# Kernel optimization log

Measured on AMD Instinct MI355X. Metric: run time of the kernel, lower is better.

## Reference

```python
import jax, jax.numpy as jnp
import numpy as np

V = 50000
E = 500000
D = 128


def setup_inputs() -> dict:
    key = jax.random.key(0)
    k1, k2, k3, k4, k5, k6 = jax.random.split(key, 6)
    edge_feats = jax.random.normal(k1, (E, D), dtype=jnp.float32)
    node_feats = jax.random.normal(k2, (V, 1), dtype=jnp.float32)
    edge_index = jax.random.randint(k3, (2, E), 0, V, dtype=jnp.int64)
    rev_index = jax.random.randint(k4, (E,), 0, E, dtype=jnp.int64)
    # Linear(hidden_dim, hidden_dim, bias=True) params, Kaiming-uniform-ish init
    lim = 1.0 / np.sqrt(D)
    W = jax.random.uniform(k5, (D, D), dtype=jnp.float32, minval=-lim, maxval=lim)
    b = jax.random.uniform(k6, (D,), dtype=jnp.float32, minval=-lim, maxval=lim)
    return {"edge_feats": edge_feats, "node_feats": node_feats, "W": W, "b": b,
            "edge_index": edge_index, "rev_index": rev_index}


def reference(edge_feats, node_feats, W, b, edge_index, rev_index):
    src, dest = edge_index[0], edge_index[1]
    messages = jax.nn.relu(edge_feats)                      # [E, d]
    # scatter-sum messages onto destination nodes
    node_messages = jax.ops.segment_sum(messages, dest, num_segments=node_feats.shape[0])  # [V, d]
    # gather back to edges, subtract reverse-edge message (D-MPNN)
    edge_messages = node_messages[src] - messages[rev_index]  # [E, d]
    # update: Linear (dropout p=0.0 is identity)
    return edge_messages @ W.T + b
```

## Files before the change

kernel.cpp:

```cpp
#include <hip/hip_runtime.h>

#define DD 128
#define TILE_E 64

typedef __attribute__((ext_vector_type(8))) short short8;
typedef __attribute__((ext_vector_type(4))) float f32x4;

__device__ __forceinline__ unsigned short f2bf(float f) {
  unsigned int u = __float_as_uint(f);
  u += 0x7FFF + ((u >> 16) & 1);
  return (unsigned short)(u >> 16);
}


__global__ __launch_bounds__(256) void hist_kernel(
    const int* __restrict__ eidx, int* __restrict__ cnt, int E) {
  int e = blockIdx.x * 256 + threadIdx.x;
  if (e < E) atomicAdd(&cnt[eidx[E + e]], 1);
}

__global__ __launch_bounds__(1024) void scan_kernel(
    const int* __restrict__ cnt, int* __restrict__ off, int* __restrict__ cur, int V) {
  __shared__ int s[1024];
  const int t = threadIdx.x;
  const int chunk = (V + 1023) / 1024;
  const int lo = t * chunk, hi = min(lo + chunk, V);
  int tot = 0;
  for (int v = lo; v < hi; ++v) tot += cnt[v];
  s[t] = tot;
  __syncthreads();
  for (int d = 1; d < 1024; d <<= 1) {
    int x = (t >= d) ? s[t - d] : 0;
    __syncthreads();
    s[t] += x;
    __syncthreads();
  }
  int run = (t > 0) ? s[t - 1] : 0;
  for (int v = lo; v < hi; ++v) {
    off[v] = run; cur[v] = run;
    run += cnt[v];
  }
}

__global__ __launch_bounds__(256) void fill_kernel(
    const int* __restrict__ eidx, int* __restrict__ cur,
    int* __restrict__ elist, int E) {
  int e = blockIdx.x * 256 + threadIdx.x;
  if (e < E) {
    int p = atomicAdd(&cur[eidx[E + e]], 1);
    elist[p] = e;
  }
}

__global__ __launch_bounds__(256) void gather_sum_kernel(
    const float* __restrict__ ef, const int* __restrict__ off,
    const int* __restrict__ cnt, const int* __restrict__ elist,
    float* __restrict__ nm, int V) {
  const int lane = threadIdx.x & 63;
  const int half = lane >> 5;
  const int l32  = lane & 31;
  const int v = blockIdx.x * 4 + (threadIdx.x >> 6);
  if (v >= V) return;
  const int base = off[v];
  const int deg  = cnt[v];
  f32x4 acc = (f32x4){0.f, 0.f, 0.f, 0.f};
  if (deg > 0) {
    const int esafe = elist[base];
    for (int j = 0; j < deg; j += 16) {
      int idx[8];
      #pragma unroll
      for (int i = 0; i < 8; ++i) {
        int sl = j + 2 * i + half;
        idx[i] = (sl < deg) ? elist[base + sl] : esafe;
      }
      const float* p0 = ef + (size_t)idx[0] * DD + l32 * 4;
      const float* p1 = ef + (size_t)idx[1] * DD + l32 * 4;
      const float* p2 = ef + (size_t)idx[2] * DD + l32 * 4;
      const float* p3 = ef + (size_t)idx[3] * DD + l32 * 4;
      const float* p4 = ef + (size_t)idx[4] * DD + l32 * 4;
      const float* p5 = ef + (size_t)idx[5] * DD + l32 * 4;
      const float* p6 = ef + (size_t)idx[6] * DD + l32 * 4;
      const float* p7 = ef + (size_t)idx[7] * DD + l32 * 4;
      float4 m0, m1, m2, m3, m4, m5, m6, m7;
      asm volatile(
          "global_load_dwordx4 %0, %8, off\n\t"
          "global_load_dwordx4 %1, %9, off\n\t"
          "global_load_dwordx4 %2, %10, off\n\t"
          "global_load_dwordx4 %3, %11, off\n\t"
          "global_load_dwordx4 %4, %12, off\n\t"
          "global_load_dwordx4 %5, %13, off\n\t"
          "global_load_dwordx4 %6, %14, off\n\t"
          "global_load_dwordx4 %7, %15, off"
          : "=&v"(m0), "=&v"(m1), "=&v"(m2), "=&v"(m3),
            "=&v"(m4), "=&v"(m5), "=&v"(m6), "=&v"(m7)
          : "v"(p0), "v"(p1), "v"(p2), "v"(p3),
            "v"(p4), "v"(p5), "v"(p6), "v"(p7)
          : "memory");
      asm volatile("s_waitcnt vmcnt(0)" ::: "memory");
      __builtin_amdgcn_sched_barrier(0);
      #pragma unroll
      for (int i = 0; i < 8; ++i) {
        float4 m;
        switch (i) {
          case 0: m = m0; break; case 1: m = m1; break;
          case 2: m = m2; break; case 3: m = m3; break;
          case 4: m = m4; break; case 5: m = m5; break;
          case 6: m = m6; break; default: m = m7; break;
        }
        int sl = j + 2 * i + half;
        if (sl < deg) {
          acc[0] += fmaxf(m.x, 0.f);
          acc[1] += fmaxf(m.y, 0.f);
          acc[2] += fmaxf(m.z, 0.f);
          acc[3] += fmaxf(m.w, 0.f);
        }
      }
    }
  }
  float4 tot;
  tot.x = acc[0] + __shfl_xor(acc[0], 32);
  tot.y = acc[1] + __shfl_xor(acc[1], 32);
  tot.z = acc[2] + __shfl_xor(acc[2], 32);
  tot.w = acc[3] + __shfl_xor(acc[3], 32);
  if (half == 0)
    ((float4*)(nm + (size_t)v * DD))[l32] = tot;
}

__global__ __launch_bounds__(256) void wconv_kernel(
    const float* __restrict__ W, unsigned short* __restrict__ Wswz) {
  int idx = blockIdx.x * 256 + threadIdx.x;
  if (idx >= DD * DD / 8) return;
  int lane = idx & 63;
  int nt   = (idx >> 6) & 7;
  int kt   = idx >> 9;
  int n = nt * 16 + (lane & 15);
  int k = kt * 32 + (lane >> 4) * 8;
  const float4* wrow = (const float4*)(W + (size_t)n * DD + k);
  float4 w0 = wrow[0];
  float4 w1 = wrow[1];
  unsigned int p0 = f2bf(w0.x) | ((unsigned int)f2bf(w0.y) << 16);
  unsigned int p1 = f2bf(w0.z) | ((unsigned int)f2bf(w0.w) << 16);
  unsigned int p2 = f2bf(w1.x) | ((unsigned int)f2bf(w1.y) << 16);
  unsigned int p3 = f2bf(w1.z) | ((unsigned int)f2bf(w1.w) << 16);
  ((uint4*)Wswz)[idx] = make_uint4(p0, p1, p2, p3);
}

__global__ __launch_bounds__(256, 4) void fused_gather_gemm_kernel(
    const float* __restrict__ ef, const float* __restrict__ nm,
    const unsigned short* __restrict__ Wswz, const float* __restrict__ bias,
    const int* __restrict__ eidx, const int* __restrict__ rev,
    float* __restrict__ out, int E) {
  const int tid  = threadIdx.x;
  const int lane = tid & 63;
  const int wave = tid >> 6;
  const int col  = lane & 15;
  const int quad = lane >> 4;
  const int e0   = blockIdx.x * TILE_E + wave * 16;

  const int ea = e0 + col;
  int s = 0, rv = 0;
  if (ea < E) { s = eidx[ea]; rv = rev[ea]; }
  const float* nb = nm + (size_t)s  * DD + quad * 8;
  const float* eb = ef + (size_t)rv * DD + quad * 8;
  const short8* __restrict__ wp = (const short8*)Wswz + lane;

  float4 a0, a1, a2, a3, a4, a5, a6, a7;
  float4 m0, m1, m2, m3, m4, m5, m6, m7;
  asm volatile(
      "global_load_dwordx4 %0, %16, off\n\t"
      "global_load_dwordx4 %1, %16, off offset:16\n\t"
      "global_load_dwordx4 %2, %17, off\n\t"
      "global_load_dwordx4 %3, %17, off offset:16\n\t"
      "global_load_dwordx4 %4, %16, off offset:128\n\t"
      "global_load_dwordx4 %5, %16, off offset:144\n\t"
      "global_load_dwordx4 %6, %17, off offset:128\n\t"
      "global_load_dwordx4 %7, %17, off offset:144\n\t"
      "global_load_dwordx4 %8, %16, off offset:256\n\t"
      "global_load_dwordx4 %9, %16, off offset:272\n\t"
      "global_load_dwordx4 %10, %17, off offset:256\n\t"
      "global_load_dwordx4 %11, %17, off offset:272\n\t"
      "global_load_dwordx4 %12, %16, off offset:384\n\t"
      "global_load_dwordx4 %13, %16, off offset:400\n\t"
      "global_load_dwordx4 %14, %17, off offset:384\n\t"
      "global_load_dwordx4 %15, %17, off offset:400"
      : "=&v"(a0), "=&v"(a1), "=&v"(m0), "=&v"(m1),
        "=&v"(a2), "=&v"(a3), "=&v"(m2), "=&v"(m3),
        "=&v"(a4), "=&v"(a5), "=&v"(m4), "=&v"(m5),
        "=&v"(a6), "=&v"(a7), "=&v"(m6), "=&v"(m7)
      : "v"(nb), "v"(eb)
      : "memory");
  asm volatile("s_waitcnt vmcnt(0)" ::: "memory");
  __builtin_amdgcn_sched_barrier(0);

  f32x4 acc[8];
  #pragma unroll
  for (int i = 0; i < 8; ++i) acc[i] = (f32x4){0.f, 0.f, 0.f, 0.f};

  #pragma unroll
  for (int kt = 0; kt < 4; ++kt) {
    float4 va0, va1, vm0, vm1;
    switch (kt) {
      case 0:  va0 = a0; va1 = a1; vm0 = m0; vm1 = m1; break;
      case 1:  va0 = a2; va1 = a3; vm0 = m2; vm1 = m3; break;
      case 2:  va0 = a4; va1 = a5; vm0 = m4; vm1 = m5; break;
      default: va0 = a6; va1 = a7; vm0 = m6; vm1 = m7; break;
    }
    float x0 = va0.x - fmaxf(vm0.x, 0.f);
    float x1 = va0.y - fmaxf(vm0.y, 0.f);
    float x2 = va0.z - fmaxf(vm0.z, 0.f);
    float x3 = va0.w - fmaxf(vm0.w, 0.f);
    float x4 = va1.x - fmaxf(vm1.x, 0.f);
    float x5 = va1.y - fmaxf(vm1.y, 0.f);
    float x6 = va1.z - fmaxf(vm1.z, 0.f);
    float x7 = va1.w - fmaxf(vm1.w, 0.f);
    union { unsigned int u[4]; short8 s8; } cvt;
    cvt.u[0] = f2bf(x0) | ((unsigned int)f2bf(x1) << 16);
    cvt.u[1] = f2bf(x2) | ((unsigned int)f2bf(x3) << 16);
    cvt.u[2] = f2bf(x4) | ((unsigned int)f2bf(x5) << 16);
    cvt.u[3] = f2bf(x6) | ((unsigned int)f2bf(x7) << 16);
    short8 av = cvt.s8;
    #pragma unroll
    for (int nt = 0; nt < 8; ++nt) {
      short8 b = wp[(kt * 8 + nt) * 64];
      acc[nt] = __builtin_amdgcn_mfma_f32_16x16x32_bf16(av, b, acc[nt], 0, 0, 0);
    }
  }

  #pragma unroll
  for (int nt = 0; nt < 8; ++nt) {
    float bj = bias[nt * 16 + col];
    #pragma unroll
    for (int r = 0; r < 4; ++r) {
      int e = e0 + quad * 4 + r;
      if (e < E)
        __builtin_nontemporal_store(acc[nt][r] + bj,
                                    &out[(size_t)e * DD + nt * 16 + col]);
    }
  }
}

extern "C" void kernel_launch(void* const* d_in, const int* in_sizes, int n_in,
                              void* d_out, int out_size, void* d_ws, size_t ws_size,
                              hipStream_t stream) {
  const float* ef   = (const float*)d_in[0];
  const float* W    = (const float*)d_in[2];
  const float* bias = (const float*)d_in[3];
  const int*   eidx = (const int*)d_in[4];
  const int*   rev  = (const int*)d_in[5];
  float*       out  = (float*)d_out;

  const int V = in_sizes[1];
  const int E = in_sizes[5];

  char* ws = (char*)d_ws;
  size_t o = 0;
  float* nm = (float*)(ws + o);            o += (size_t)V * DD * sizeof(float);
  o = (o + 255) & ~(size_t)255;
  int* cnt  = (int*)(ws + o);              o += (size_t)V * sizeof(int);
  o = (o + 255) & ~(size_t)255;
  int* off  = (int*)(ws + o);              o += (size_t)V * sizeof(int);
  o = (o + 255) & ~(size_t)255;
  int* cur  = (int*)(ws + o);              o += (size_t)V * sizeof(int);
  o = (o + 255) & ~(size_t)255;
  int* elist = (int*)(ws + o);             o += (size_t)E * sizeof(int);
  o = (o + 255) & ~(size_t)255;
  unsigned short* Wswz = (unsigned short*)(ws + o);

  hipMemsetAsync(cnt, 0, (size_t)V * sizeof(int), stream);

  int eb = (E + 255) / 256;
  hist_kernel<<<eb, 256, 0, stream>>>(eidx, cnt, E);
  scan_kernel<<<1, 1024, 0, stream>>>(cnt, off, cur, V);
  fill_kernel<<<eb, 256, 0, stream>>>(eidx, cur, elist, E);
  gather_sum_kernel<<<(V + 3) / 4, 256, 0, stream>>>(ef, off, cnt, elist, nm, V);
  wconv_kernel<<<(DD * DD / 8 + 255) / 256, 256, 0, stream>>>(W, Wswz);

  int nblocks = (E + TILE_E - 1) / TILE_E;
  fused_gather_gemm_kernel<<<nblocks, 256, 0, stream>>>(ef, nm, Wswz, bias, eidx, rev, out, E);
}
```

Before: 714.1 us.

## Write bf16 relu messages in scatter pass and parallelize scan with wave shuffles

During the node gather-sum, each visited edge's relu message is also written out as packed bf16, so the final GEMM kernel reads the reverse-edge message at half the bytes and without reapplying relu. The single-block scan is replaced by a chunked wave-shuffle scan, which reads cnt in a coalesced way instead of each thread walking a serial chunk. This adds a 128 MB-class bf16 write stream in the gather kernel and rounds the reverse message to bf16 before the subtraction. Edges whose destination is counted are each written exactly once, so every message gets written.

New measurement: 667.0 us. 6.6% less time.

```diff
diff --git a/kernel.cpp b/kernel.cpp
--- a/kernel.cpp
+++ b/kernel.cpp
@@ -21,24 +21,42 @@
 
 __global__ __launch_bounds__(1024) void scan_kernel(
     const int* __restrict__ cnt, int* __restrict__ off, int* __restrict__ cur, int V) {
-  __shared__ int s[1024];
-  const int t = threadIdx.x;
-  const int chunk = (V + 1023) / 1024;
-  const int lo = t * chunk, hi = min(lo + chunk, V);
-  int tot = 0;
-  for (int v = lo; v < hi; ++v) tot += cnt[v];
-  s[t] = tot;
+  __shared__ int wsum[16];
+  __shared__ int woff[16];
+  __shared__ int carry;
+  const int t    = threadIdx.x;
+  const int lane = t & 63;
+  const int wid  = t >> 6;
+  if (t == 0) carry = 0;
   __syncthreads();
-  for (int d = 1; d < 1024; d <<= 1) {
-    int x = (t >= d) ? s[t - d] : 0;
-    __syncthreads();
-    s[t] += x;
-    __syncthreads();
-  }
-  int run = (t > 0) ? s[t - 1] : 0;
-  for (int v = lo; v < hi; ++v) {
-    off[v] = run; cur[v] = run;
-    run += cnt[v];
+  for (int base = 0; base < V; base += 1024) {
+    int i = base + t;
+    int x = (i < V) ? cnt[i] : 0;
+    int v = x;
+    #pragma unroll
+    for (int d = 1; d < 64; d <<= 1) {
+      int y = __shfl_up(v, d);
+      if (lane >= d) v += y;
+    }
+    if (lane == 63) wsum[wid] = v;
+    __syncthreads();
+    if (wid == 0) {
+      int wv = (lane < 16) ? wsum[lane] : 0;
+      #pragma unroll
+      for (int d = 1; d < 16; d <<= 1) {
+        int y = __shfl_up(wv, d);
+        if (lane >= d) wv += y;
+      }
+      if (lane < 16) woff[lane] = wv;
+    }
+    __syncthreads();
+    int wexcl = (wid > 0) ? woff[wid - 1] : 0;
+    int excl  = carry + wexcl + v - x;
+    if (i < V) { off[i] = excl; cur[i] = excl; }
+    int tot = woff[15];
+    __syncthreads();
+    if (t == 0) carry += tot;
+    __syncthreads();
   }
 }
 
@@ -55,7 +73,7 @@
 __global__ __launch_bounds__(256) void gather_sum_kernel(
     const float* __restrict__ ef, const int* __restrict__ off,
     const int* __restrict__ cnt, const int* __restrict__ elist,
-    float* __restrict__ nm, int V) {
+    float* __restrict__ nm, unsigned short* __restrict__ mbf, int V) {
   const int lane = threadIdx.x & 63;
   const int half = lane >> 5;
   const int l32  = lane & 31;
@@ -109,10 +127,15 @@
         }
         int sl = j + 2 * i + half;
         if (sl < deg) {
-          acc[0] += fmaxf(m.x, 0.f);
-          acc[1] += fmaxf(m.y, 0.f);
-          acc[2] += fmaxf(m.z, 0.f);
-          acc[3] += fmaxf(m.w, 0.f);
+          float r0 = fmaxf(m.x, 0.f);
+          float r1 = fmaxf(m.y, 0.f);
+          float r2 = fmaxf(m.z, 0.f);
+          float r3 = fmaxf(m.w, 0.f);
+          acc[0] += r0; acc[1] += r1; acc[2] += r2; acc[3] += r3;
+          uint2 pk;
+          pk.x = f2bf(r0) | ((unsigned int)f2bf(r1) << 16);
+          pk.y = f2bf(r2) | ((unsigned int)f2bf(r3) << 16);
+          *(uint2*)(mbf + (size_t)idx[i] * DD + l32 * 4) = pk;
         }
       }
     }
@@ -146,7 +169,7 @@
 }
 
 __global__ __launch_bounds__(256, 4) void fused_gather_gemm_kernel(
-    const float* __restrict__ ef, const float* __restrict__ nm,
+    const float* __restrict__ nm, const unsigned short* __restrict__ mbf,
     const unsigned short* __restrict__ Wswz, const float* __restrict__ bias,
     const int* __restrict__ eidx, const int* __restrict__ rev,
     float* __restrict__ out, int E) {
@@ -160,36 +183,20 @@
   const int ea = e0 + col;
   int s = 0, rv = 0;
   if (ea < E) { s = eidx[ea]; rv = rev[ea]; }
-  const float* nb = nm + (size_t)s  * DD + quad * 8;
-  const float* eb = ef + (size_t)rv * DD + quad * 8;
+  const float4* __restrict__ nmp = (const float4*)(nm + (size_t)s * DD);
+  const uint4*  __restrict__ mp  = (const uint4*)(mbf + (size_t)rv * DD);
+
   const short8* __restrict__ wp = (const short8*)Wswz + lane;
 
-  float4 a0, a1, a2, a3, a4, a5, a6, a7;
-  float4 m0, m1, m2, m3, m4, m5, m6, m7;
-  asm volatile(
-      "global_load_dwordx4 %0, %16, off\n\t"
-      "global_load_dwordx4 %1, %16, off offset:16\n\t"
-      "global_load_dwordx4 %2, %17, off\n\t"
-      "global_load_dwordx4 %3, %17, off offset:16\n\t"
-      "global_load_dwordx4 %4, %16, off offset:128\n\t"
-      "global_load_dwordx4 %5, %16, off offset:144\n\t"
-      "global_load_dwordx4 %6, %17, off offset:128\n\t"
-      "global_load_dwordx4 %7, %17, off offset:144\n\t"
-      "global_load_dwordx4 %8, %16, off offset:256\n\t"
-      "global_load_dwordx4 %9, %16, off offset:272\n\t"
-      "global_load_dwordx4 %10, %17, off offset:256\n\t"
-      "global_load_dwordx4 %11, %17, off offset:272\n\t"
-      "global_load_dwordx4 %12, %16, off offset:384\n\t"
-      "global_load_dwordx4 %13, %16, off offset:400\n\t"
-      "global_load_dwordx4 %14, %17, off offset:384\n\t"
-      "global_load_dwordx4 %15, %17, off offset:400"
-      : "=&v"(a0), "=&v"(a1), "=&v"(m0), "=&v"(m1),
-        "=&v"(a2), "=&v"(a3), "=&v"(m2), "=&v"(m3),
-        "=&v"(a4), "=&v"(a5), "=&v"(m4), "=&v"(m5),
-        "=&v"(a6), "=&v"(a7), "=&v"(m6), "=&v"(m7)
-      : "v"(nb), "v"(eb)
-      : "memory");
-  asm volatile("s_waitcnt vmcnt(0)" ::: "memory");
+  float4 a[8];
+  uint4  mm[4];
+  #pragma unroll
+  for (int kt = 0; kt < 4; ++kt) {
+    const int k4 = kt * 8 + quad * 2;
+    a[kt * 2]     = nmp[k4];
+    a[kt * 2 + 1] = nmp[k4 + 1];
+    mm[kt]        = mp[kt * 4 + quad];
+  }
   __builtin_amdgcn_sched_barrier(0);
 
   f32x4 acc[8];
@@ -198,26 +205,21 @@
 
   #pragma unroll
   for (int kt = 0; kt < 4; ++kt) {
-    float4 va0, va1, vm0, vm1;
-    switch (kt) {
-      case 0:  va0 = a0; va1 = a1; vm0 = m0; vm1 = m1; break;
-      case 1:  va0 = a2; va1 = a3; vm0 = m2; vm1 = m3; break;
-      case 2:  va0 = a4; va1 = a5; vm0 = m4; vm1 = m5; break;
-      default: va0 = a6; va1 = a7; vm0 = m6; vm1 = m7; break;
-    }
-    float x0 = va0.x - fmaxf(vm0.x, 0.f);
-    float x1 = va0.y - fmaxf(vm0.y, 0.f);
-    float x2 = va0.z - fmaxf(vm0.z, 0.f);
-    float x3 = va0.w - fmaxf(vm0.w, 0.f);
-    float x4 = va1.x - fmaxf(vm1.x, 0.f);
-    float x5 = va1.y - fmaxf(vm1.y, 0.f);
-    float x6 = va1.z - fmaxf(vm1.z, 0.f);
-    float x7 = va1.w - fmaxf(vm1.w, 0.f);
-    union { unsigned int u[4]; short8 s8; } cvt;
-    cvt.u[0] = f2bf(x0) | ((unsigned int)f2bf(x1) << 16);
-    cvt.u[1] = f2bf(x2) | ((unsigned int)f2bf(x3) << 16);
-    cvt.u[2] = f2bf(x4) | ((unsigned int)f2bf(x5) << 16);
-    cvt.u[3] = f2bf(x6) | ((unsigned int)f2bf(x7) << 16);
+    float4 a0 = a[kt * 2], a1 = a[kt * 2 + 1];
+    uint4  u  = mm[kt];
+    float x0 = a0.x - __uint_as_float(u.x << 16);
+    float x1 = a0.y - __uint_as_float(u.x & 0xFFFF0000u);
+    float x2 = a0.z - __uint_as_float(u.y << 16);
+    float x3 = a0.w - __uint_as_float(u.y & 0xFFFF0000u);
+    float x4 = a1.x - __uint_as_float(u.z << 16);
+    float x5 = a1.y - __uint_as_float(u.z & 0xFFFF0000u);
+    float x6 = a1.z - __uint_as_float(u.w << 16);
+    float x7 = a1.w - __uint_as_float(u.w & 0xFFFF0000u);
+    union { unsigned int uu[4]; short8 s8; } cvt;
+    cvt.uu[0] = f2bf(x0) | ((unsigned int)f2bf(x1) << 16);
+    cvt.uu[1] = f2bf(x2) | ((unsigned int)f2bf(x3) << 16);
+    cvt.uu[2] = f2bf(x4) | ((unsigned int)f2bf(x5) << 16);
+    cvt.uu[3] = f2bf(x6) | ((unsigned int)f2bf(x7) << 16);
     short8 av = cvt.s8;
     #pragma unroll
     for (int nt = 0; nt < 8; ++nt) {
@@ -265,6 +267,9 @@
   int* elist = (int*)(ws + o);             o += (size_t)E * sizeof(int);
   o = (o + 255) & ~(size_t)255;
   unsigned short* Wswz = (unsigned short*)(ws + o);
+  o += (size_t)DD * DD * sizeof(unsigned short);
+  o = (o + 255) & ~(size_t)255;
+  unsigned short* mbf = (unsigned short*)(ws + o);
 
   hipMemsetAsync(cnt, 0, (size_t)V * sizeof(int), stream);
 
@@ -272,9 +277,9 @@
   hist_kernel<<<eb, 256, 0, stream>>>(eidx, cnt, E);
   scan_kernel<<<1, 1024, 0, stream>>>(cnt, off, cur, V);
   fill_kernel<<<eb, 256, 0, stream>>>(eidx, cur, elist, E);
-  gather_sum_kernel<<<(V + 3) / 4, 256, 0, stream>>>(ef, off, cnt, elist, nm, V);
+  gather_sum_kernel<<<(V + 3) / 4, 256, 0, stream>>>(ef, off, cnt, elist, nm, mbf, V);
   wconv_kernel<<<(DD * DD / 8 + 255) / 256, 256, 0, stream>>>(W, Wswz);
 
   int nblocks = (E + TILE_E - 1) / TILE_E;
-  fused_gather_gemm_kernel<<<nblocks, 256, 0, stream>>>(ef, nm, Wswz, bias, eidx, rev, out, E);
-}
+  fused_gather_gemm_kernel<<<nblocks, 256, 0, stream>>>(nm, mbf, Wswz, bias, eidx, rev, out, E);
+}
```
